# Optimization experiments

Measured on AMD Instinct MI355X. Metric: run time of the kernel, lower is better.

## Reference

```python
import jax, jax.numpy as jnp
import numpy as np

SAMPLING_RATE = 0.5

def setup_inputs() -> dict:
    key = jax.random.key(0)
    k1, k2 = jax.random.split(key)
    token = jax.random.normal(k1, (8, 16, 4, 384), dtype=jnp.float32)
    feature = jax.random.normal(k2, (8, 16, 4, 196, 384), dtype=jnp.float32)
    return {"token": token, "feature": feature}

def reference(token, feature):
    b1, n1, kk1, c = token.shape
    b2, n2, kk2, hw, _ = feature.shape
    N = n1 * kk1  # == n2 * kk2
    tok = token.reshape(b1, N, 1, c)           # [b, N, 1, c]
    feat = feature.reshape(b2, N, hw, c)       # [b, N, hw, c]
    scale = c ** (-0.5)
    # attention scores: [b, N, 1, hw]
    attn = jnp.einsum('bnqc,bnhc->bnqh', tok, feat) * scale
    attn = jax.nn.softmax(attn, axis=-1)
    tk = int(hw * SAMPLING_RATE)
    sel_attn, sel_idx = jax.lax.top_k(attn, tk)          # [b, N, 1, tk]
    sel_attn = sel_attn / jnp.sum(sel_attn, axis=-1, keepdims=True)
    # gather selected features: idx [b, N, tk] -> feat rows [b, N, tk, c]
    idx = sel_idx[:, :, 0, :]                            # [b, N, tk]
    sel_feat = jnp.take_along_axis(feat, idx[..., None], axis=2)  # [b, N, tk, c]
    out = jnp.einsum('bnqt,bntc->bnqc', sel_attn, sel_feat)       # [b, N, 1, c]
    return out.reshape(b1, n1, kk1, c)
```

## Files before the change

kernel.cpp:

```cpp
#include <hip/hip_runtime.h>

#define HW 196
#define C  384
#define CF4 (C/4)
#define TK 98
#define NT 512
#define NWAVE (NT/64)

__global__ __launch_bounds__(NT, 4) void sampling_kernel(
    const float* __restrict__ token,
    const float* __restrict__ feature,
    float* __restrict__ out)
{
    __shared__ float tokLds[C];
    __shared__ float score[HW];
    __shared__ float selW[TK];
    __shared__ int   selIdx[TK];
    __shared__ float wsum[NWAVE];
    __shared__ int   rank2[2 * HW];
    __shared__ float part[NWAVE][C];
    __shared__ float s_max, s_winv;

    const int tid  = threadIdx.x;
    const int wave = tid >> 6;
    const int lane = tid & 63;
    const int l8   = lane & 7;
    const int g8   = lane >> 3;
    const int pair = blockIdx.x;

    const float* tokp  = token   + (size_t)pair * C;
    const float* featp = feature + (size_t)pair * (HW * C);
    const float4* f4base = (const float4*)featp;
    const float4* t4     = (const float4*)tokLds;

    for (int i = tid; i < C; i += NT) tokLds[i] = tokp[i];
    __syncthreads();

    float4 tok[12];
    #pragma unroll
    for (int k = 0; k < 12; ++k) tok[k] = t4[l8 + 8 * k];

    const float scale = 0.05103103630798288f;

    #pragma unroll
    for (int it = 0; it < 3; ++it) {
        const int r = it * 64 + wave * 8 + g8;
        const float4* fr = f4base + (size_t)r * CF4 + l8;
        float4 a[12];
        #pragma unroll
        for (int k = 0; k < 12; ++k) a[k] = fr[8 * k];
        float4 acc = make_float4(0.f, 0.f, 0.f, 0.f);
        #pragma unroll
        for (int k = 0; k < 12; ++k) {
            acc.x += a[k].x * tok[k].x; acc.y += a[k].y * tok[k].y;
            acc.z += a[k].z * tok[k].z; acc.w += a[k].w * tok[k].w;
        }
        float s = (acc.x + acc.y) + (acc.z + acc.w);
        s += __shfl_xor(s, 1, 64);
        s += __shfl_xor(s, 2, 64);
        s += __shfl_xor(s, 4, 64);
        if (l8 == 0) score[r] = s * scale;
    }
    if (wave < 4 && g8 == 0) {
        const int r = 192 + wave;
        const float4* fr = f4base + (size_t)r * CF4 + l8;
        float4 acc = make_float4(0.f, 0.f, 0.f, 0.f);
        #pragma unroll
        for (int k = 0; k < 12; ++k) {
            float4 a = fr[8 * k];
            acc.x += a.x * tok[k].x; acc.y += a.y * tok[k].y;
            acc.z += a.z * tok[k].z; acc.w += a.w * tok[k].w;
        }
        float s = (acc.x + acc.y) + (acc.z + acc.w);
        s += __shfl_xor(s, 1, 64);
        s += __shfl_xor(s, 2, 64);
        s += __shfl_xor(s, 4, 64);
        if (l8 == 0) score[r] = s * scale;
    }
    __syncthreads();

    if (tid < 2 * HW) {
        const int i = tid >> 1, h = tid & 1;
        const float si = score[i];
        int cnt = 0;
        const int j0 = h * (HW / 2);
        for (int j = j0; j < j0 + HW / 2; ++j) {
            const float sj = score[j];
            cnt += (int)((sj > si) | ((sj == si) & (j < i)));
        }
        rank2[tid] = cnt;
    } else if (wave == NWAVE - 1) {
        float m = -3.4e38f;
        for (int i = lane; i < HW; i += 64) m = fmaxf(m, score[i]);
        #pragma unroll
        for (int off = 32; off > 0; off >>= 1)
            m = fmaxf(m, __shfl_xor(m, off, 64));
        if (lane == 0) s_max = m;
    }
    __syncthreads();

    float w = 0.f;
    if (tid < HW) {
        const int rank = rank2[2 * tid] + rank2[2 * tid + 1];
        if (rank < TK) {
            w = __expf(score[tid] - s_max);
            selIdx[rank] = tid;
            selW[rank]  = w;
        }
    }
    #pragma unroll
    for (int off = 32; off > 0; off >>= 1) w += __shfl_xor(w, off, 64);
    if (lane == 0) wsum[wave] = w;
    __syncthreads();
    if (tid == 0) {
        float s = 0.f;
        #pragma unroll
        for (int i = 0; i < NWAVE; ++i) s += wsum[i];
        s_winv = 1.f / s;
    }
    __syncthreads();

    float4 acc_a = make_float4(0.f, 0.f, 0.f, 0.f);
    float4 acc_b = make_float4(0.f, 0.f, 0.f, 0.f);
    #pragma unroll
    for (int j = 0; j < 12; ++j) {
        const int i = wave + NWAVE * j;
        const int   r   = selIdx[i];
        const float wgt = selW[i];
        const float4* f4 = f4base + (size_t)r * CF4;
        float4 aa = f4[lane];
        acc_a.x += wgt * aa.x; acc_a.y += wgt * aa.y;
        acc_a.z += wgt * aa.z; acc_a.w += wgt * aa.w;
        if (lane < 32) {
            float4 bb = f4[64 + lane];
            acc_b.x += wgt * bb.x; acc_b.y += wgt * bb.y;
            acc_b.z += wgt * bb.z; acc_b.w += wgt * bb.w;
        }
    }
    if (wave < TK - 96) {
        const int i = 96 + wave;
        const int   r   = selIdx[i];
        const float wgt = selW[i];
        const float4* f4 = f4base + (size_t)r * CF4;
        float4 aa = f4[lane];
        acc_a.x += wgt * aa.x; acc_a.y += wgt * aa.y;
        acc_a.z += wgt * aa.z; acc_a.w += wgt * aa.w;
        if (lane < 32) {
            float4 bb = f4[64 + lane];
            acc_b.x += wgt * bb.x; acc_b.y += wgt * bb.y;
            acc_b.z += wgt * bb.z; acc_b.w += wgt * bb.w;
        }
    }
    float4* pw = (float4*)&part[wave][0];
    pw[lane] = acc_a;
    if (lane < 32) pw[64 + lane] = acc_b;
    __syncthreads();

    if (tid < C) {
        float s = 0.f;
        #pragma unroll
        for (int wv = 0; wv < NWAVE; ++wv) s += part[wv][tid];
        out[(size_t)pair * C + tid] = s * s_winv;
    }
}

extern "C" void kernel_launch(void* const* d_in, const int* in_sizes, int n_in,
                              void* d_out, int out_size, void* d_ws, size_t ws_size,
                              hipStream_t stream) {
    const float* token   = (const float*)d_in[0];
    const float* feature = (const float*)d_in[1];
    float* out = (float*)d_out;
    const int pairs = in_sizes[0] / C;
    sampling_kernel<<<pairs, NT, 0, stream>>>(token, feature, out);
}
```

Before: 38.11 us.

## Cache feature rows in LDS as fp16 and gather from shared memory

```diff
diff --git a/kernel.cpp b/kernel.cpp
--- a/kernel.cpp
+++ b/kernel.cpp
@@ -1,10 +1,11 @@
 #include <hip/hip_runtime.h>
+#include <hip/hip_fp16.h>
 
 #define HW 196
 #define C  384
 #define CF4 (C/4)
 #define TK 98
-#define NT 512
+#define NT 1024
 #define NWAVE (NT/64)
 
 __global__ __launch_bounds__(NT, 4) void sampling_kernel(
@@ -12,13 +13,14 @@
     const float* __restrict__ feature,
     float* __restrict__ out)
 {
+    __shared__ __half feat16[HW][C];
     __shared__ float tokLds[C];
     __shared__ float score[HW];
     __shared__ float selW[TK];
     __shared__ int   selIdx[TK];
     __shared__ float wsum[NWAVE];
     __shared__ int   rank2[2 * HW];
-    __shared__ float part[NWAVE][C];
+    __shared__ float part2[2][C];
     __shared__ float s_max, s_winv;
 
     const int tid  = threadIdx.x;
@@ -43,39 +45,31 @@
     const float scale = 0.05103103630798288f;
 
     #pragma unroll
-    for (int it = 0; it < 3; ++it) {
-        const int r = it * 64 + wave * 8 + g8;
-        const float4* fr = f4base + (size_t)r * CF4 + l8;
-        float4 a[12];
-        #pragma unroll
-        for (int k = 0; k < 12; ++k) a[k] = fr[8 * k];
-        float4 acc = make_float4(0.f, 0.f, 0.f, 0.f);
-        #pragma unroll
-        for (int k = 0; k < 12; ++k) {
-            acc.x += a[k].x * tok[k].x; acc.y += a[k].y * tok[k].y;
-            acc.z += a[k].z * tok[k].z; acc.w += a[k].w * tok[k].w;
+    for (int it = 0; it < 2; ++it) {
+        const int r = it * 128 + wave * 8 + g8;
+        if (r < HW) {
+            const float4* fr = f4base + (size_t)r * CF4 + l8;
+            float4 a[12];
+            #pragma unroll
+            for (int k = 0; k < 12; ++k) a[k] = fr[8 * k];
+            float4 acc = make_float4(0.f, 0.f, 0.f, 0.f);
+            #pragma unroll
+            for (int k = 0; k < 12; ++k) {
+                acc.x += a[k].x * tok[k].x; acc.y += a[k].y * tok[k].y;
+                acc.z += a[k].z * tok[k].z; acc.w += a[k].w * tok[k].w;
+            }
+            #pragma unroll
+            for (int k = 0; k < 12; ++k) {
+                const int c0 = l8 * 4 + 32 * k;
+                *(__half2*)&feat16[r][c0]     = __floats2half2_rn(a[k].x, a[k].y);
+                *(__half2*)&feat16[r][c0 + 2] = __floats2half2_rn(a[k].z, a[k].w);
+            }
+            float s = (acc.x + acc.y) + (acc.z + acc.w);
+            s += __shfl_xor(s, 1, 64);
+            s += __shfl_xor(s, 2, 64);
+            s += __shfl_xor(s, 4, 64);
+            if (l8 == 0) score[r] = s * scale;
         }
-        float s = (acc.x + acc.y) + (acc.z + acc.w);
-        s += __shfl_xor(s, 1, 64);
-        s += __shfl_xor(s, 2, 64);
-        s += __shfl_xor(s, 4, 64);
-        if (l8 == 0) score[r] = s * scale;
-    }
-    if (wave < 4 && g8 == 0) {
-        const int r = 192 + wave;
-        const float4* fr = f4base + (size_t)r * CF4 + l8;
-        float4 acc = make_float4(0.f, 0.f, 0.f, 0.f);
-        #pragma unroll
-        for (int k = 0; k < 12; ++k) {
-            float4 a = fr[8 * k];
-            acc.x += a.x * tok[k].x; acc.y += a.y * tok[k].y;
-            acc.z += a.z * tok[k].z; acc.w += a.w * tok[k].w;
-        }
-        float s = (acc.x + acc.y) + (acc.z + acc.w);
-        s += __shfl_xor(s, 1, 64);
-        s += __shfl_xor(s, 2, 64);
-        s += __shfl_xor(s, 4, 64);
-        if (l8 == 0) score[r] = s * scale;
     }
     __syncthreads();
 
@@ -120,48 +114,21 @@
     }
     __syncthreads();
 
-    float4 acc_a = make_float4(0.f, 0.f, 0.f, 0.f);
-    float4 acc_b = make_float4(0.f, 0.f, 0.f, 0.f);
-    #pragma unroll
-    for (int j = 0; j < 12; ++j) {
-        const int i = wave + NWAVE * j;
-        const int   r   = selIdx[i];
-        const float wgt = selW[i];
-        const float4* f4 = f4base + (size_t)r * CF4;
-        float4 aa = f4[lane];
-        acc_a.x += wgt * aa.x; acc_a.y += wgt * aa.y;
-        acc_a.z += wgt * aa.z; acc_a.w += wgt * aa.w;
-        if (lane < 32) {
-            float4 bb = f4[64 + lane];
-            acc_b.x += wgt * bb.x; acc_b.y += wgt * bb.y;
-            acc_b.z += wgt * bb.z; acc_b.w += wgt * bb.w;
-        }
+    if (tid < 2 * C) {
+        const int h = tid >> 8 >= 1 ? (tid >= C ? 1 : 0) : 0;
+        const int hh = (tid >= C) ? 1 : 0;
+        const int c  = tid - hh * C;
+        float acc = 0.f;
+        #pragma unroll 7
+        for (int i = hh; i < TK; i += 2)
+            acc += selW[i] * __half2float(feat16[selIdx[i]][c]);
+        part2[hh][c] = acc;
+        (void)h;
     }
-    if (wave < TK - 96) {
-        const int i = 96 + wave;
-        const int   r   = selIdx[i];
-        const float wgt = selW[i];
-        const float4* f4 = f4base + (size_t)r * CF4;
-        float4 aa = f4[lane];
-        acc_a.x += wgt * aa.x; acc_a.y += wgt * aa.y;
-        acc_a.z += wgt * aa.z; acc_a.w += wgt * aa.w;
-        if (lane < 32) {
-            float4 bb = f4[64 + lane];
-            acc_b.x += wgt * bb.x; acc_b.y += wgt * bb.y;
-            acc_b.z += wgt * bb.z; acc_b.w += wgt * bb.w;
-        }
-    }
-    float4* pw = (float4*)&part[wave][0];
-    pw[lane] = acc_a;
-    if (lane < 32) pw[64 + lane] = acc_b;
     __syncthreads();
 
-    if (tid < C) {
-        float s = 0.f;
-        #pragma unroll
-        for (int wv = 0; wv < NWAVE; ++wv) s += part[wv][tid];
-        out[(size_t)pair * C + tid] = s * s_winv;
-    }
+    if (tid < C)
+        out[(size_t)pair * C + tid] = (part2[0][tid] + part2[1][tid]) * s_winv;
 }
 
 extern "C" void kernel_launch(void* const* d_in, const int* in_sizes, int n_in,
```

New measurement: 40.44 us. 6.1% more time.

## Split score computation into separate wide-grid kernel writing scores to workspace

Applied to the files above, without the earlier changes.

```diff
diff --git a/kernel.cpp b/kernel.cpp
--- a/kernel.cpp
+++ b/kernel.cpp
@@ -4,15 +4,61 @@
 #define C  384
 #define CF4 (C/4)
 #define TK 98
+#define SLICES 7
+#define RPS 28
+
+__global__ __launch_bounds__(256) void score_kernel(
+    const float* __restrict__ token,
+    const float* __restrict__ feature,
+    float* __restrict__ scores)
+{
+    __shared__ float4 tokLds[CF4];
+
+    const int tid   = threadIdx.x;
+    const int bid   = blockIdx.x;
+    const int pair  = bid / SLICES;
+    const int slice = bid - pair * SLICES;
+    const int g     = tid >> 3;
+    const int l8    = tid & 7;
+
+    const float* tokp = token + (size_t)pair * C;
+    const float4* f4base = (const float4*)(feature + (size_t)pair * (HW * C));
+
+    if (tid < CF4) tokLds[tid] = ((const float4*)tokp)[tid];
+    __syncthreads();
+
+    const bool active = (g < RPS);
+    const int  r = slice * RPS + g;
+    const float4* fr = f4base + (size_t)r * CF4 + l8;
+
+    float4 a[12];
+    if (active) {
+        #pragma unroll
+        for (int k = 0; k < 12; ++k) a[k] = fr[8 * k];
+        float4 acc = make_float4(0.f, 0.f, 0.f, 0.f);
+        #pragma unroll
+        for (int k = 0; k < 12; ++k) {
+            float4 t = tokLds[l8 + 8 * k];
+            acc.x += a[k].x * t.x; acc.y += a[k].y * t.y;
+            acc.z += a[k].z * t.z; acc.w += a[k].w * t.w;
+        }
+        float s = (acc.x + acc.y) + (acc.z + acc.w);
+        s += __shfl_xor(s, 1, 64);
+        s += __shfl_xor(s, 2, 64);
+        s += __shfl_xor(s, 4, 64);
+        if (l8 == 0)
+            scores[(size_t)pair * HW + r] = s * 0.05103103630798288f;
+    }
+}
+
 #define NT 512
 #define NWAVE (NT/64)
 
-__global__ __launch_bounds__(NT, 4) void sampling_kernel(
-    const float* __restrict__ token,
+__global__ __launch_bounds__(NT) void select_kernel(
     const float* __restrict__ feature,
+    const float* __restrict__ scores_g,
     float* __restrict__ out)
 {
-    __shared__ float tokLds[C];
     __shared__ float score[HW];
     __shared__ float selW[TK];
     __shared__ int   selIdx[TK];
@@ -24,59 +70,11 @@
     const int tid  = threadIdx.x;
     const int wave = tid >> 6;
     const int lane = tid & 63;
-    const int l8   = lane & 7;
-    const int g8   = lane >> 3;
     const int pair = blockIdx.x;
 
-    const float* tokp  = token   + (size_t)pair * C;
-    const float* featp = feature + (size_t)pair * (HW * C);
-    const float4* f4base = (const float4*)featp;
-    const float4* t4     = (const float4*)tokLds;
+    const float4* f4base = (const float4*)(feature + (size_t)pair * (HW * C));
 
-    for (int i = tid; i < C; i += NT) tokLds[i] = tokp[i];
-    __syncthreads();
-
-    float4 tok[12];
-    #pragma unroll
-    for (int k = 0; k < 12; ++k) tok[k] = t4[l8 + 8 * k];
-
-    const float scale = 0.05103103630798288f;
-
-    #pragma unroll
-    for (int it = 0; it < 3; ++it) {
-        const int r = it * 64 + wave * 8 + g8;
-        const float4* fr = f4base + (size_t)r * CF4 + l8;
-        float4 a[12];
-        #pragma unroll
-        for (int k = 0; k < 12; ++k) a[k] = fr[8 * k];
-        float4 acc = make_float4(0.f, 0.f, 0.f, 0.f);
-        #pragma unroll
-        for (int k = 0; k < 12; ++k) {
-            acc.x += a[k].x * tok[k].x; acc.y += a[k].y * tok[k].y;
-            acc.z += a[k].z * tok[k].z; acc.w += a[k].w * tok[k].w;
-        }
-        float s = (acc.x + acc.y) + (acc.z + acc.w);
-        s += __shfl_xor(s, 1, 64);
-        s += __shfl_xor(s, 2, 64);
-        s += __shfl_xor(s, 4, 64);
-        if (l8 == 0) score[r] = s * scale;
-    }
-    if (wave < 4 && g8 == 0) {
-        const int r = 192 + wave;
-        const float4* fr = f4base + (size_t)r * CF4 + l8;
-        float4 acc = make_float4(0.f, 0.f, 0.f, 0.f);
-        #pragma unroll
-        for (int k = 0; k < 12; ++k) {
-            float4 a = fr[8 * k];
-            acc.x += a.x * tok[k].x; acc.y += a.y * tok[k].y;
-            acc.z += a.z * tok[k].z; acc.w += a.w * tok[k].w;
-        }
-        float s = (acc.x + acc.y) + (acc.z + acc.w);
-        s += __shfl_xor(s, 1, 64);
-        s += __shfl_xor(s, 2, 64);
-        s += __shfl_xor(s, 4, 64);
-        if (l8 == 0) score[r] = s * scale;
-    }
+    if (tid < HW) score[tid] = scores_g[(size_t)pair * HW + tid];
     __syncthreads();
 
     if (tid < 2 * HW) {
@@ -169,7 +167,10 @@
                               hipStream_t stream) {
     const float* token   = (const float*)d_in[0];
     const float* feature = (const float*)d_in[1];
-    float* out = (float*)d_out;
+    float* out    = (float*)d_out;
+    float* scores = (float*)d_ws;
     const int pairs = in_sizes[0] / C;
-    sampling_kernel<<<pairs, NT, 0, stream>>>(token, feature, out);
+
+    score_kernel<<<pairs * SLICES, 256, 0, stream>>>(token, feature, scores);
+    select_kernel<<<pairs, NT, 0, stream>>>(feature, scores, out);
 }
```

Result: slower. 45.04 us (+18.2%).

## Halve block size, read token from LDS, and fuse rank with max computation

Applied to the files above, without the earlier changes.

```diff
diff --git a/kernel.cpp b/kernel.cpp
--- a/kernel.cpp
+++ b/kernel.cpp
@@ -4,47 +4,40 @@
 #define C  384
 #define CF4 (C/4)
 #define TK 98
-#define NT 512
+#define NT 256
 #define NWAVE (NT/64)
 
-__global__ __launch_bounds__(NT, 4) void sampling_kernel(
+__global__ __launch_bounds__(NT) void sampling_kernel(
     const float* __restrict__ token,
     const float* __restrict__ feature,
     float* __restrict__ out)
 {
-    __shared__ float tokLds[C];
+    __shared__ float4 tokLds[CF4];
     __shared__ float score[HW];
     __shared__ float selW[TK];
     __shared__ int   selIdx[TK];
     __shared__ float wsum[NWAVE];
-    __shared__ int   rank2[2 * HW];
     __shared__ float part[NWAVE][C];
-    __shared__ float s_max, s_winv;
+    __shared__ float s_winv;
 
     const int tid  = threadIdx.x;
     const int wave = tid >> 6;
     const int lane = tid & 63;
     const int l8   = lane & 7;
-    const int g8   = lane >> 3;
+    const int grp  = tid >> 3;
     const int pair = blockIdx.x;
 
-    const float* tokp  = token   + (size_t)pair * C;
-    const float* featp = feature + (size_t)pair * (HW * C);
-    const float4* f4base = (const float4*)featp;
-    const float4* t4     = (const float4*)tokLds;
+    const float* tokp = token + (size_t)pair * C;
+    const float4* f4base = (const float4*)(feature + (size_t)pair * (HW * C));
 
-    for (int i = tid; i < C; i += NT) tokLds[i] = tokp[i];
+    if (tid < CF4) tokLds[tid] = ((const float4*)tokp)[tid];
     __syncthreads();
-
-    float4 tok[12];
-    #pragma unroll
-    for (int k = 0; k < 12; ++k) tok[k] = t4[l8 + 8 * k];
 
     const float scale = 0.05103103630798288f;
 
     #pragma unroll
-    for (int it = 0; it < 3; ++it) {
-        const int r = it * 64 + wave * 8 + g8;
+    for (int it = 0; it < 6; ++it) {
+        const int r = it * 32 + grp;
         const float4* fr = f4base + (size_t)r * CF4 + l8;
         float4 a[12];
         #pragma unroll
@@ -52,8 +45,9 @@
         float4 acc = make_float4(0.f, 0.f, 0.f, 0.f);
         #pragma unroll
         for (int k = 0; k < 12; ++k) {
-            acc.x += a[k].x * tok[k].x; acc.y += a[k].y * tok[k].y;
-            acc.z += a[k].z * tok[k].z; acc.w += a[k].w * tok[k].w;
+            float4 t = tokLds[l8 + 8 * k];
+            acc.x += a[k].x * t.x; acc.y += a[k].y * t.y;
+            acc.z += a[k].z * t.z; acc.w += a[k].w * t.w;
         }
         float s = (acc.x + acc.y) + (acc.z + acc.w);
         s += __shfl_xor(s, 1, 64);
@@ -61,15 +55,16 @@
         s += __shfl_xor(s, 4, 64);
         if (l8 == 0) score[r] = s * scale;
     }
-    if (wave < 4 && g8 == 0) {
-        const int r = 192 + wave;
+    if (grp < 4) {
+        const int r = 192 + grp;
         const float4* fr = f4base + (size_t)r * CF4 + l8;
         float4 acc = make_float4(0.f, 0.f, 0.f, 0.f);
         #pragma unroll
         for (int k = 0; k < 12; ++k) {
             float4 a = fr[8 * k];
-            acc.x += a.x * tok[k].x; acc.y += a.y * tok[k].y;
-            acc.z += a.z * tok[k].z; acc.w += a.w * tok[k].w;
+            float4 t = tokLds[l8 + 8 * k];
+            acc.x += a.x * t.x; acc.y += a.y * t.y;
+            acc.z += a.z * t.z; acc.w += a.w * t.w;
         }
         float s = (acc.x + acc.y) + (acc.z + acc.w);
         s += __shfl_xor(s, 1, 64);
@@ -79,31 +74,18 @@
     }
     __syncthreads();
 
-    if (tid < 2 * HW) {
-        const int i = tid >> 1, h = tid & 1;
-        const float si = score[i];
-        int cnt = 0;
-        const int j0 = h * (HW / 2);
-        for (int j = j0; j < j0 + HW / 2; ++j) {
-            const float sj = score[j];
-            cnt += (int)((sj > si) | ((sj == si) & (j < i)));
-        }
-        rank2[tid] = cnt;
-    } else if (wave == NWAVE - 1) {
-        float m = -3.4e38f;
-        for (int i = lane; i < HW; i += 64) m = fmaxf(m, score[i]);
-        #pragma unroll
-        for (int off = 32; off > 0; off >>= 1)
-            m = fmaxf(m, __shfl_xor(m, off, 64));
-        if (lane == 0) s_max = m;
-    }
-    __syncthreads();
-
     float w = 0.f;
     if (tid < HW) {
-        const int rank = rank2[2 * tid] + rank2[2 * tid + 1];
+        const float si = score[tid];
+        int   rank = 0;
+        float m    = -3.4e38f;
+        for (int j = 0; j < HW; ++j) {
+            const float sj = score[j];
+            rank += (int)((sj > si) | ((sj == si) & (j < tid)));
+            m = fmaxf(m, sj);
+        }
         if (rank < TK) {
-            w = __expf(score[tid] - s_max);
+            w = __expf(si - m);
             selIdx[rank] = tid;
             selW[rank]  = w;
         }
@@ -112,18 +94,14 @@
     for (int off = 32; off > 0; off >>= 1) w += __shfl_xor(w, off, 64);
     if (lane == 0) wsum[wave] = w;
     __syncthreads();
-    if (tid == 0) {
-        float s = 0.f;
-        #pragma unroll
-        for (int i = 0; i < NWAVE; ++i) s += wsum[i];
-        s_winv = 1.f / s;
-    }
+    if (tid == 0)
+        s_winv = 1.f / (wsum[0] + wsum[1] + wsum[2] + wsum[3]);
     __syncthreads();
 
     float4 acc_a = make_float4(0.f, 0.f, 0.f, 0.f);
     float4 acc_b = make_float4(0.f, 0.f, 0.f, 0.f);
     #pragma unroll
-    for (int j = 0; j < 12; ++j) {
+    for (int j = 0; j < 24; ++j) {
         const int i = wave + NWAVE * j;
         const int   r   = selIdx[i];
         const float wgt = selW[i];
@@ -156,11 +134,9 @@
     if (lane < 32) pw[64 + lane] = acc_b;
     __syncthreads();
 
-    if (tid < C) {
-        float s = 0.f;
-        #pragma unroll
-        for (int wv = 0; wv < NWAVE; ++wv) s += part[wv][tid];
-        out[(size_t)pair * C + tid] = s * s_winv;
+    for (int c = tid; c < C; c += NT) {
+        float s = (part[0][c] + part[1][c]) + (part[2][c] + part[3][c]);
+        out[(size_t)pair * C + c] = s * s_winv;
     }
 }
 
```

Result: slower. 43.15 us (+13.2%).
